# Kernel optimization log

Hardware: AMD Instinct MI355X
Metric: run time of the kernel (lower is better)

## Reference

```python
import jax, jax.numpy as jnp
import numpy as np

N = 100000      # nodes
E = 1600000     # edges (before self-loops)
F_IN = 128      # dataset.num_node_features
H, C = 8, 8     # heads, hid
D = H * C       # 64, concat output dim
G = 64          # graphs in batch
N_CLS = 10
SLOPE = 0.2     # PyG GATConv negative_slope default


def setup_inputs() -> dict:
    key = jax.random.key(0)
    ks = jax.random.split(key, 16)
    s = 0.1
    return {
        "x": jax.random.normal(ks[0], (N, F_IN), jnp.float32),
        "edge_index": jax.random.randint(ks[1], (2, E), 0, N, jnp.int32),
        "batch": jnp.sort(jax.random.randint(ks[2], (N,), 0, G, jnp.int32)),
        "W1": jax.random.normal(ks[3], (F_IN, D), jnp.float32) * s,
        "a1_src": jax.random.normal(ks[4], (H, C), jnp.float32) * s,
        "a1_dst": jax.random.normal(ks[5], (H, C), jnp.float32) * s,
        "b1": jnp.zeros((D,), jnp.float32),
        "W2": jax.random.normal(ks[6], (D, D), jnp.float32) * s,
        "a2_src": jax.random.normal(ks[7], (H, C), jnp.float32) * s,
        "a2_dst": jax.random.normal(ks[8], (H, C), jnp.float32) * s,
        "b2": jnp.zeros((D,), jnp.float32),
        "W3": jax.random.normal(ks[9], (D, D), jnp.float32) * s,
        "a3_src": jax.random.normal(ks[10], (H, C), jnp.float32) * s,
        "a3_dst": jax.random.normal(ks[11], (H, C), jnp.float32) * s,
        "b3": jnp.zeros((D,), jnp.float32),
        "lin_W": jax.random.normal(ks[12], (D, N_CLS), jnp.float32) * s,
        "lin_b": jnp.zeros((N_CLS,), jnp.float32),
    }


def _gat_conv(h_in, src, dst, W, a_src, a_dst, b):
    # h: [N, H, C] per-head projected features
    h = (h_in @ W).reshape(N, H, C)
    al_src = jnp.einsum('nhc,hc->nh', h, a_src)  # [N, H]
    al_dst = jnp.einsum('nhc,hc->nh', h, a_dst)
    e = al_src[src] + al_dst[dst]                # [E', H]
    e = jnp.where(e > 0, e, SLOPE * e)           # LeakyReLU
    # segment softmax over incoming edges of each dst node
    m = jax.ops.segment_max(e, dst, num_segments=N)          # every node has a self-loop
    e = jnp.exp(e - m[dst])
    denom = jax.ops.segment_sum(e, dst, num_segments=N)
    alpha = e / denom[dst]                        # [E', H]
    out = jax.ops.segment_sum(h[src] * alpha[:, :, None], dst, num_segments=N)
    return out.reshape(N, D) + b


def reference(x, edge_index, batch, W1, a1_src, a1_dst, b1,
              W2, a2_src, a2_dst, b2, W3, a3_src, a3_dst, b3, lin_W, lin_b):
    # PyG GATConv add_self_loops=True
    loop = jnp.arange(N, dtype=edge_index.dtype)
    src = jnp.concatenate([edge_index[0], loop])
    dst = jnp.concatenate([edge_index[1], loop])

    h = jax.nn.elu(_gat_conv(x, src, dst, W1, a1_src, a1_dst, b1))
    h = jax.nn.elu(_gat_conv(h, src, dst, W2, a2_src, a2_dst, b2))
    h = jax.nn.elu(_gat_conv(h, src, dst, W3, a3_src, a3_dst, b3))

    # global mean pool over graph assignment
    sums = jax.ops.segment_sum(h, batch, num_segments=G)          # [G, D]
    cnts = jax.ops.segment_sum(jnp.ones((N,), h.dtype), batch, num_segments=G)
    pooled = sums / jnp.maximum(cnts, 1.0)[:, None]

    return pooled @ lin_W + lin_b  # [G, N_CLS]
```

## Files before the change

### kernel.cpp

```cpp
#include <hip/hip_runtime.h>
#include <math.h>

#define NN 100000
#define EE 1600000
#define GG 64
#define NCLS 10

#define BSH 8
#define NB 391
#define BCAP 4608
#define EPS 4096
#define CAPS 5120

typedef unsigned int uint32;

__device__ __forceinline__ unsigned short f2bf(float f) {
    unsigned u = __float_as_uint(f);
    unsigned r = (u + 0x7fffu + ((u >> 16) & 1u)) >> 16;
    return (unsigned short)r;
}


__global__ __launch_bounds__(512) void bscatter_kernel(
    const int* __restrict__ src, const int* __restrict__ dst,
    int* __restrict__ bfill, uint32* __restrict__ bpack, int n) {
    __shared__ int hist[512], gbase[512], lbase[512], cnt2[512];
    __shared__ int wtot[8];
    __shared__ uint32 lsd[EPS];
    __shared__ unsigned short bkt[EPS];
    int tid = threadIdx.x;
    int lane = tid & 63, wv = tid >> 6;
    int e0 = blockIdx.x * EPS;
    int e1 = min(e0 + EPS, n);

    hist[tid] = 0;
    cnt2[tid] = 0;
    __syncthreads();
    for (int e = e0 + tid; e < e1; e += 512) atomicAdd(&hist[dst[e] >> BSH], 1);
    __syncthreads();
    int h = hist[tid];
    int inc = h;
#pragma unroll
    for (int off = 1; off < 64; off <<= 1) {
        int t = __shfl_up(inc, off);
        if (lane >= off) inc += t;
    }
    if (lane == 63) wtot[wv] = inc;
    __syncthreads();
    if (tid < 8) {
        int t = wtot[tid];
#pragma unroll
        for (int off = 1; off < 8; off <<= 1) {
            int u = __shfl_up(t, off, 8);
            if (tid >= off) t += u;
        }
        wtot[tid] = t;
    }
    __syncthreads();
    if (wv > 0) inc += wtot[wv - 1];
    int lb = inc - h;
    lbase[tid] = lb;
    int go = h > 0 ? atomicAdd(&bfill[tid], h) : 0;
    gbase[tid] = tid * BCAP + go - lb;
    __syncthreads();
    for (int e = e0 + tid; e < e1; e += 512) {
        int s = src[e], dd = dst[e];
        int b = dd >> BSH;
        int r = atomicAdd(&cnt2[b], 1);
        int slot = lbase[b] + r;
        lsd[slot] = ((uint32)s << 8) | (uint32)(dd & 255);
        bkt[slot] = (unsigned short)b;
    }
    __syncthreads();
    int m = e1 - e0;
    for (int i = tid; i < m; i += 512)
        bpack[gbase[bkt[i]] + i] = lsd[i];
}

__global__ __launch_bounds__(256) void bsort_kernel(
    const uint32* __restrict__ bpack, const int* __restrict__ bfill,
    int* __restrict__ rp, int* __restrict__ re, int* __restrict__ col) {
    __shared__ int cnt[256], cnt2[256];
    __shared__ int wtot[4];
    __shared__ int stage[CAPS];
    int b = blockIdx.x;
    int tid = threadIdx.x;
    int ebeg = b * BCAP;
    int sz = bfill[b];
    int n0 = b << BSH;
    int nn = min(256, NN - n0);

    cnt[tid] = 0;
    cnt2[tid] = 0;
    __syncthreads();
    const uint4* bq = (const uint4*)(bpack + ebeg);
    int nq = sz >> 2;
    for (int i = tid; i < nq; i += 256) {
        uint4 p = bq[i];
        atomicAdd(&cnt[p.x & 255u], 1);
        atomicAdd(&cnt[p.y & 255u], 1);
        atomicAdd(&cnt[p.z & 255u], 1);
        atomicAdd(&cnt[p.w & 255u], 1);
    }
    for (int e = (nq << 2) + tid; e < sz; e += 256)
        atomicAdd(&cnt[bpack[ebeg + e] & 255u], 1);
    __syncthreads();
    int lane = tid & 63, wv = tid >> 6;
    int c = cnt[tid];
    int inc = c;
#pragma unroll
    for (int off = 1; off < 64; off <<= 1) {
        int t = __shfl_up(inc, off);
        if (lane >= off) inc += t;
    }
    if (lane == 63) wtot[wv] = inc;
    __syncthreads();
    if (tid < 4) {
        int t = wtot[tid];
#pragma unroll
        for (int off = 1; off < 4; off <<= 1) {
            int u = __shfl_up(t, off, 4);
            if (tid >= off) t += u;
        }
        wtot[tid] = t;
    }
    __syncthreads();
    if (wv > 0) inc += wtot[wv - 1];
    int excl = inc - c;
    cnt[tid] = excl;
    if (tid < nn) {
        rp[n0 + tid] = ebeg + excl;
        re[n0 + tid] = ebeg + inc;
    }
    __syncthreads();
    bool fits = sz <= CAPS;
    for (int i = tid; i < nq; i += 256) {
        uint4 p = bq[i];
        int d0 = (int)(p.x & 255u), d1 = (int)(p.y & 255u);
        int d2 = (int)(p.z & 255u), d3 = (int)(p.w & 255u);
        int p0 = cnt[d0] + atomicAdd(&cnt2[d0], 1);
        int p1 = cnt[d1] + atomicAdd(&cnt2[d1], 1);
        int p2 = cnt[d2] + atomicAdd(&cnt2[d2], 1);
        int p3 = cnt[d3] + atomicAdd(&cnt2[d3], 1);
        if (fits) {
            stage[p0] = (int)(p.x >> 8); stage[p1] = (int)(p.y >> 8);
            stage[p2] = (int)(p.z >> 8); stage[p3] = (int)(p.w >> 8);
        } else {
            col[ebeg + p0] = (int)(p.x >> 8); col[ebeg + p1] = (int)(p.y >> 8);
            col[ebeg + p2] = (int)(p.z >> 8); col[ebeg + p3] = (int)(p.w >> 8);
        }
    }
    for (int e = (nq << 2) + tid; e < sz; e += 256) {
        uint32 p = bpack[ebeg + e];
        int dl = (int)(p & 255u);
        int pos = cnt[dl] + atomicAdd(&cnt2[dl], 1);
        if (fits) stage[pos] = (int)(p >> 8);
        else col[ebeg + pos] = (int)(p >> 8);
    }
    __syncthreads();
    if (fits) {
        uint4* colq = (uint4*)(col + ebeg);
        const uint4* stq = (const uint4*)stage;
        for (int i = tid; i < nq; i += 256) colq[i] = stq[i];
        for (int i = (nq << 2) + tid; i < sz; i += 256) col[ebeg + i] = stage[i];
    }
}


template <int K>
__global__ __launch_bounds__(256) void gemm_al_kernel(
    const float* __restrict__ X, const float* __restrict__ W,
    const float* __restrict__ a_src, const float* __restrict__ a_dst,
    unsigned short* __restrict__ H, float* __restrict__ ALs, float* __restrict__ ALd,
    int nrows) {
    const int KC = 64;
    const int KP = KC + 4;
    __shared__ float Xs[64 * (KC + 4)];
    __shared__ float Ws[K * 64];
    int tid = threadIdx.x;
    int r0 = blockIdx.x * 64;
    int validRows = min(64, nrows - r0);

    {
        const float4* Wg = (const float4*)W;
        float4* Ws4 = (float4*)Ws;
        for (int i = tid; i < K * 16; i += 256) Ws4[i] = Wg[i];
    }

    int cg = tid & 15, rg = tid >> 4;
    int rbase = rg * 4;
    float4 acc0 = make_float4(0.f, 0.f, 0.f, 0.f);
    float4 acc1 = acc0, acc2 = acc0, acc3 = acc0;

    const float4* Xg = (const float4*)X;
    const int QG = K / 4;

    for (int kc = 0; kc < K; kc += KC) {
        __syncthreads();
        for (int i = tid; i < 64 * 16; i += 256) {
            int row = i >> 4, q = i & 15;
            float4 v = (row < validRows)
                ? Xg[(size_t)(r0 + row) * QG + (kc >> 2) + q]
                : make_float4(0.f, 0.f, 0.f, 0.f);
            *(float4*)&Xs[row * KP + q * 4] = v;
        }
        __syncthreads();

#pragma unroll 2
        for (int k = 0; k < KC; k += 4) {
            float4 x0 = *(const float4*)&Xs[(rbase + 0) * KP + k];
            float4 x1 = *(const float4*)&Xs[(rbase + 1) * KP + k];
            float4 x2 = *(const float4*)&Xs[(rbase + 2) * KP + k];
            float4 x3 = *(const float4*)&Xs[(rbase + 3) * KP + k];
            float4 w0 = *(const float4*)&Ws[(kc + k + 0) * 64 + 4 * cg];
            float4 w1 = *(const float4*)&Ws[(kc + k + 1) * 64 + 4 * cg];
            float4 w2 = *(const float4*)&Ws[(kc + k + 2) * 64 + 4 * cg];
            float4 w3 = *(const float4*)&Ws[(kc + k + 3) * 64 + 4 * cg];
#define FMA4(A, S, WV) \
            A.x = fmaf(S, WV.x, A.x); A.y = fmaf(S, WV.y, A.y); \
            A.z = fmaf(S, WV.z, A.z); A.w = fmaf(S, WV.w, A.w)
            FMA4(acc0, x0.x, w0); FMA4(acc1, x1.x, w0); FMA4(acc2, x2.x, w0); FMA4(acc3, x3.x, w0);
            FMA4(acc0, x0.y, w1); FMA4(acc1, x1.y, w1); FMA4(acc2, x2.y, w1); FMA4(acc3, x3.y, w1);
            FMA4(acc0, x0.z, w2); FMA4(acc1, x1.z, w2); FMA4(acc2, x2.z, w2); FMA4(acc3, x3.z, w2);
            FMA4(acc0, x0.w, w3); FMA4(acc1, x1.w, w3); FMA4(acc2, x2.w, w3); FMA4(acc3, x3.w, w3);
#undef FMA4
        }
    }

    int hh = cg >> 1;
    float4 as4 = ((const float4*)a_src)[cg];
    float4 ad4 = ((const float4*)a_dst)[cg];
    float4 accs[4] = {acc0, acc1, acc2, acc3};
#pragma unroll
    for (int i = 0; i < 4; ++i) {
        int r = r0 + rbase + i;
        if (r < nrows) {
            ushort4 p;
            p.x = f2bf(accs[i].x); p.y = f2bf(accs[i].y);
            p.z = f2bf(accs[i].z); p.w = f2bf(accs[i].w);
            ((ushort4*)H)[(size_t)r * 16 + cg] = p;
            float ps = accs[i].x * as4.x + accs[i].y * as4.y +
                       accs[i].z * as4.z + accs[i].w * as4.w;
            float pd = accs[i].x * ad4.x + accs[i].y * ad4.y +
                       accs[i].z * ad4.z + accs[i].w * ad4.w;
            ps += __shfl_xor(ps, 1);
            pd += __shfl_xor(pd, 1);
            if ((cg & 1) == 0) {
                ALs[r * 8 + hh] = ps;
                ALd[r * 8 + hh] = pd;
            }
        }
    }
}


__global__ __launch_bounds__(256, 6) void agg_kernel(
    const unsigned short* __restrict__ H, const float* __restrict__ ALs,
    const float* __restrict__ ALd, const int* __restrict__ rp,
    const int* __restrict__ re, const int* __restrict__ col,
    const float* __restrict__ bias, float* __restrict__ Out, int n) {
    int tid = threadIdx.x;
    int lane = tid & 63;
    int slot = lane >> 3, head = lane & 7;
    int wid = blockIdx.x * 4 + (tid >> 6);
    int d = wid * 8 + slot;
    bool active = d < n;
    if (!active) d = n - 1;
    const uint4* __restrict__ Hq = (const uint4*)H;

    float ad = ALd[d * 8 + head];
    float acc0 = 0.f, acc1 = 0.f, acc2 = 0.f, acc3 = 0.f;
    float acc4 = 0.f, acc5 = 0.f, acc6 = 0.f, acc7 = 0.f;
    float wsum = 0.f;

#define FMA8(U, W) { \
    acc0 = fmaf(W, __uint_as_float((U).x << 16), acc0); \
    acc1 = fmaf(W, __uint_as_float((U).x & 0xffff0000u), acc1); \
    acc2 = fmaf(W, __uint_as_float((U).y << 16), acc2); \
    acc3 = fmaf(W, __uint_as_float((U).y & 0xffff0000u), acc3); \
    acc4 = fmaf(W, __uint_as_float((U).z << 16), acc4); \
    acc5 = fmaf(W, __uint_as_float((U).z & 0xffff0000u), acc5); \
    acc6 = fmaf(W, __uint_as_float((U).w << 16), acc6); \
    acc7 = fmaf(W, __uint_as_float((U).w & 0xffff0000u), acc7); }

    {
        uint4 u = Hq[(size_t)d * 8 + head];
        float e = ALs[d * 8 + head] + ad;
        e = fmaxf(e, 0.2f * e);
        float w = __expf(e);
        FMA8(u, w);
        wsum = w;
    }

    int k = rp[d], kend = re[d];
    for (; k + 4 <= kend; k += 4) {
        int s0 = col[k], s1 = col[k + 1], s2 = col[k + 2], s3 = col[k + 3];
        uint4 u0 = Hq[(size_t)s0 * 8 + head];
        uint4 u1 = Hq[(size_t)s1 * 8 + head];
        uint4 u2 = Hq[(size_t)s2 * 8 + head];
        uint4 u3 = Hq[(size_t)s3 * 8 + head];
        float a0 = ALs[s0 * 8 + head];
        float a1 = ALs[s1 * 8 + head];
        float a2 = ALs[s2 * 8 + head];
        float a3 = ALs[s3 * 8 + head];
        float e0 = a0 + ad; e0 = fmaxf(e0, 0.2f * e0); float w0 = __expf(e0);
        float e1 = a1 + ad; e1 = fmaxf(e1, 0.2f * e1); float w1 = __expf(e1);
        float e2 = a2 + ad; e2 = fmaxf(e2, 0.2f * e2); float w2 = __expf(e2);
        float e3 = a3 + ad; e3 = fmaxf(e3, 0.2f * e3); float w3 = __expf(e3);
        FMA8(u0, w0);
        FMA8(u1, w1);
        FMA8(u2, w2);
        FMA8(u3, w3);
        wsum += (w0 + w1) + (w2 + w3);
    }
    if (k + 2 <= kend) {
        int s0 = col[k], s1 = col[k + 1];
        uint4 u0 = Hq[(size_t)s0 * 8 + head];
        uint4 u1 = Hq[(size_t)s1 * 8 + head];
        float a0 = ALs[s0 * 8 + head];
        float a1 = ALs[s1 * 8 + head];
        float e0 = a0 + ad; e0 = fmaxf(e0, 0.2f * e0); float w0 = __expf(e0);
        float e1 = a1 + ad; e1 = fmaxf(e1, 0.2f * e1); float w1 = __expf(e1);
        FMA8(u0, w0);
        FMA8(u1, w1);
        wsum += w0 + w1;
        k += 2;
    }
    if (k < kend) {
        int s = col[k];
        uint4 u = Hq[(size_t)s * 8 + head];
        float a = ALs[s * 8 + head];
        float e = a + ad; e = fmaxf(e, 0.2f * e);
        float w = __expf(e);
        FMA8(u, w);
        wsum += w;
    }
#undef FMA8

    if (active) {
        float inv = 1.f / wsum;
        float4 b0 = ((const float4*)bias)[head * 2];
        float4 b1 = ((const float4*)bias)[head * 2 + 1];
        float4 o0, o1;
        o0.x = fmaf(acc0, inv, b0.x); o0.x = o0.x > 0.f ? o0.x : expm1f(o0.x);
        o0.y = fmaf(acc1, inv, b0.y); o0.y = o0.y > 0.f ? o0.y : expm1f(o0.y);
        o0.z = fmaf(acc2, inv, b0.z); o0.z = o0.z > 0.f ? o0.z : expm1f(o0.z);
        o0.w = fmaf(acc3, inv, b0.w); o0.w = o0.w > 0.f ? o0.w : expm1f(o0.w);
        o1.x = fmaf(acc4, inv, b1.x); o1.x = o1.x > 0.f ? o1.x : expm1f(o1.x);
        o1.y = fmaf(acc5, inv, b1.y); o1.y = o1.y > 0.f ? o1.y : expm1f(o1.y);
        o1.z = fmaf(acc6, inv, b1.z); o1.z = o1.z > 0.f ? o1.z : expm1f(o1.z);
        o1.w = fmaf(acc7, inv, b1.w); o1.w = o1.w > 0.f ? o1.w : expm1f(o1.w);
        ((float4*)Out)[(size_t)d * 16 + head * 2] = o0;
        ((float4*)Out)[(size_t)d * 16 + head * 2 + 1] = o1;
    }
}


__global__ void pool_kernel(const float* __restrict__ H, const int* __restrict__ batch,
                            float* __restrict__ sums, float* __restrict__ cnt, int n) {
    int gw = (int)((blockIdx.x * blockDim.x + threadIdx.x) >> 6);
    int lane = threadIdx.x & 63;
    int n0 = gw * 64;
    if (n0 >= n) return;
    int n1 = min(n0 + 64, n);
    int curb = batch[n0];
    float local = 0.f, c_local = 0.f;
    for (int i = n0; i < n1; ++i) {
        int b = batch[i];
        if (b != curb) {
            atomicAdd(&sums[curb * 64 + lane], local);
            if (lane == 0) atomicAdd(&cnt[curb], c_local);
            local = 0.f;
            c_local = 0.f;
            curb = b;
        }
        local += H[(size_t)i * 64 + lane];
        c_local += 1.f;
    }
    atomicAdd(&sums[curb * 64 + lane], local);
    if (lane == 0) atomicAdd(&cnt[curb], c_local);
}

__global__ void final_kernel(const float* __restrict__ sums, const float* __restrict__ cnt,
                             const float* __restrict__ W, const float* __restrict__ b,
                             float* __restrict__ out) {
    int t = blockIdx.x * blockDim.x + threadIdx.x;
    if (t >= GG * NCLS) return;
    int g = t / NCLS, k = t % NCLS;
    float c = cnt[g];
    if (c < 1.f) c = 1.f;
    float inv = 1.f / c;
    float acc = b[k];
#pragma unroll
    for (int cc = 0; cc < 64; ++cc)
        acc = fmaf(sums[g * 64 + cc] * inv, W[cc * NCLS + k], acc);
    out[t] = acc;
}


extern "C" void kernel_launch(void* const* d_in, const int* in_sizes, int n_in,
                              void* d_out, int out_size, void* d_ws, size_t ws_size,
                              hipStream_t stream) {
    const float* x    = (const float*)d_in[0];
    const int*   ei   = (const int*)d_in[1];
    const int*   batch = (const int*)d_in[2];
    const float* W1 = (const float*)d_in[3];
    const float* a1s = (const float*)d_in[4];
    const float* a1d = (const float*)d_in[5];
    const float* b1 = (const float*)d_in[6];
    const float* W2 = (const float*)d_in[7];
    const float* a2s = (const float*)d_in[8];
    const float* a2d = (const float*)d_in[9];
    const float* b2 = (const float*)d_in[10];
    const float* W3 = (const float*)d_in[11];
    const float* a3s = (const float*)d_in[12];
    const float* a3d = (const float*)d_in[13];
    const float* b3 = (const float*)d_in[14];
    const float* linW = (const float*)d_in[15];
    const float* linb = (const float*)d_in[16];
    float* out = (float*)d_out;

    char* ws = (char*)d_ws;
    size_t off = 0;
    auto alloc = [&](size_t bytes) -> void* {
        void* p = ws + off;
        off = (off + bytes + 255) & ~(size_t)255;
        return p;
    };
    unsigned short* hBf = (unsigned short*)alloc((size_t)NN * 64 * 2);
    float* hF     = (float*)alloc((size_t)NN * 64 * 4);
    float* ALs    = (float*)alloc((size_t)NN * 8 * 4);
    float* ALd    = (float*)alloc((size_t)NN * 8 * 4);
    int*   rp     = (int*)alloc((size_t)NN * 4);
    int*   reArr  = (int*)alloc((size_t)NN * 4);
    int*   bfill  = (int*)alloc((size_t)NB * 4);
    uint32* bpack = (uint32*)alloc((size_t)NB * BCAP * 4);
    int*   col    = (int*)alloc((size_t)NB * BCAP * 4);
    float* sums   = (float*)alloc((size_t)(GG * 64 + GG) * 4);
    float* gcnt   = sums + GG * 64;

    const int NBLK = (NN + 255) / 256;
    const int SB = (EE + EPS - 1) / EPS;

    hipMemsetAsync(bfill, 0, (size_t)NB * 4, stream);
    bscatter_kernel<<<SB, 512, 0, stream>>>(ei, ei + EE, bfill, bpack, EE);
    bsort_kernel<<<NB, 256, 0, stream>>>(bpack, bfill, rp, reArr, col);

    const int GB = (NN + 63) / 64;
    const int AB = (NN + 31) / 32;

    gemm_al_kernel<128><<<GB, 256, 0, stream>>>(x, W1, a1s, a1d, hBf, ALs, ALd, NN);
    agg_kernel<<<AB, 256, 0, stream>>>(hBf, ALs, ALd, rp, reArr, col, b1, hF, NN);

    gemm_al_kernel<64><<<GB, 256, 0, stream>>>(hF, W2, a2s, a2d, hBf, ALs, ALd, NN);
    agg_kernel<<<AB, 256, 0, stream>>>(hBf, ALs, ALd, rp, reArr, col, b2, hF, NN);

    gemm_al_kernel<64><<<GB, 256, 0, stream>>>(hF, W3, a3s, a3d, hBf, ALs, ALd, NN);
    agg_kernel<<<AB, 256, 0, stream>>>(hBf, ALs, ALd, rp, reArr, col, b3, hF, NN);

    hipMemsetAsync(sums, 0, (size_t)(GG * 64 + GG) * 4, stream);
    pool_kernel<<<NBLK, 256, 0, stream>>>(hF, batch, sums, gcnt, NN);
    final_kernel<<<3, 256, 0, stream>>>(sums, gcnt, linW, linb, out);
}
```

Measured before the change: 395.7 us.

## Fuse aggregation with next-layer GEMM, merge scatter with first GEMM, fuse pooling

The edge bucket scatter and the first-layer projection GEMM now run as one launch, with blocks partitioned by role so they can overlap. Each layer's attention aggregation writes its ELU output into shared memory, and the next layer's projection and attention logits are computed from it, so the fp32 hidden tensor no longer round-trips through global memory. The last layer fuses aggregation with mean pooling and uses a last-block ticket to run the final linear layer. Row pointers are packed into int2, and H/AL buffers are ping-ponged between layers. Fewer launches and less memory traffic are traded for lower occupancy in the fused blocks (more shared memory per block) and atomic ticket synchronisation.

```diff
diff --git a/kernel.cpp b/kernel.cpp
--- a/kernel.cpp
+++ b/kernel.cpp
@@ -11,6 +11,8 @@
 #define BCAP 4608
 #define EPS 4096
 #define CAPS 5120
+#define SBLK 391
+#define GB 1563
 
 typedef unsigned int uint32;
 
@@ -21,253 +23,11 @@
 }
 
 
-__global__ __launch_bounds__(512) void bscatter_kernel(
-    const int* __restrict__ src, const int* __restrict__ dst,
-    int* __restrict__ bfill, uint32* __restrict__ bpack, int n) {
-    __shared__ int hist[512], gbase[512], lbase[512], cnt2[512];
-    __shared__ int wtot[8];
-    __shared__ uint32 lsd[EPS];
-    __shared__ unsigned short bkt[EPS];
-    int tid = threadIdx.x;
-    int lane = tid & 63, wv = tid >> 6;
-    int e0 = blockIdx.x * EPS;
-    int e1 = min(e0 + EPS, n);
-
-    hist[tid] = 0;
-    cnt2[tid] = 0;
-    __syncthreads();
-    for (int e = e0 + tid; e < e1; e += 512) atomicAdd(&hist[dst[e] >> BSH], 1);
-    __syncthreads();
-    int h = hist[tid];
-    int inc = h;
-#pragma unroll
-    for (int off = 1; off < 64; off <<= 1) {
-        int t = __shfl_up(inc, off);
-        if (lane >= off) inc += t;
-    }
-    if (lane == 63) wtot[wv] = inc;
-    __syncthreads();
-    if (tid < 8) {
-        int t = wtot[tid];
-#pragma unroll
-        for (int off = 1; off < 8; off <<= 1) {
-            int u = __shfl_up(t, off, 8);
-            if (tid >= off) t += u;
-        }
-        wtot[tid] = t;
-    }
-    __syncthreads();
-    if (wv > 0) inc += wtot[wv - 1];
-    int lb = inc - h;
-    lbase[tid] = lb;
-    int go = h > 0 ? atomicAdd(&bfill[tid], h) : 0;
-    gbase[tid] = tid * BCAP + go - lb;
-    __syncthreads();
-    for (int e = e0 + tid; e < e1; e += 512) {
-        int s = src[e], dd = dst[e];
-        int b = dd >> BSH;
-        int r = atomicAdd(&cnt2[b], 1);
-        int slot = lbase[b] + r;
-        lsd[slot] = ((uint32)s << 8) | (uint32)(dd & 255);
-        bkt[slot] = (unsigned short)b;
-    }
-    __syncthreads();
-    int m = e1 - e0;
-    for (int i = tid; i < m; i += 512)
-        bpack[gbase[bkt[i]] + i] = lsd[i];
-}
-
-__global__ __launch_bounds__(256) void bsort_kernel(
-    const uint32* __restrict__ bpack, const int* __restrict__ bfill,
-    int* __restrict__ rp, int* __restrict__ re, int* __restrict__ col) {
-    __shared__ int cnt[256], cnt2[256];
-    __shared__ int wtot[4];
-    __shared__ int stage[CAPS];
-    int b = blockIdx.x;
-    int tid = threadIdx.x;
-    int ebeg = b * BCAP;
-    int sz = bfill[b];
-    int n0 = b << BSH;
-    int nn = min(256, NN - n0);
-
-    cnt[tid] = 0;
-    cnt2[tid] = 0;
-    __syncthreads();
-    const uint4* bq = (const uint4*)(bpack + ebeg);
-    int nq = sz >> 2;
-    for (int i = tid; i < nq; i += 256) {
-        uint4 p = bq[i];
-        atomicAdd(&cnt[p.x & 255u], 1);
-        atomicAdd(&cnt[p.y & 255u], 1);
-        atomicAdd(&cnt[p.z & 255u], 1);
-        atomicAdd(&cnt[p.w & 255u], 1);
-    }
-    for (int e = (nq << 2) + tid; e < sz; e += 256)
-        atomicAdd(&cnt[bpack[ebeg + e] & 255u], 1);
-    __syncthreads();
-    int lane = tid & 63, wv = tid >> 6;
-    int c = cnt[tid];
-    int inc = c;
-#pragma unroll
-    for (int off = 1; off < 64; off <<= 1) {
-        int t = __shfl_up(inc, off);
-        if (lane >= off) inc += t;
-    }
-    if (lane == 63) wtot[wv] = inc;
-    __syncthreads();
-    if (tid < 4) {
-        int t = wtot[tid];
-#pragma unroll
-        for (int off = 1; off < 4; off <<= 1) {
-            int u = __shfl_up(t, off, 4);
-            if (tid >= off) t += u;
-        }
-        wtot[tid] = t;
-    }
-    __syncthreads();
-    if (wv > 0) inc += wtot[wv - 1];
-    int excl = inc - c;
-    cnt[tid] = excl;
-    if (tid < nn) {
-        rp[n0 + tid] = ebeg + excl;
-        re[n0 + tid] = ebeg + inc;
-    }
-    __syncthreads();
-    bool fits = sz <= CAPS;
-    for (int i = tid; i < nq; i += 256) {
-        uint4 p = bq[i];
-        int d0 = (int)(p.x & 255u), d1 = (int)(p.y & 255u);
-        int d2 = (int)(p.z & 255u), d3 = (int)(p.w & 255u);
-        int p0 = cnt[d0] + atomicAdd(&cnt2[d0], 1);
-        int p1 = cnt[d1] + atomicAdd(&cnt2[d1], 1);
-        int p2 = cnt[d2] + atomicAdd(&cnt2[d2], 1);
-        int p3 = cnt[d3] + atomicAdd(&cnt2[d3], 1);
-        if (fits) {
-            stage[p0] = (int)(p.x >> 8); stage[p1] = (int)(p.y >> 8);
-            stage[p2] = (int)(p.z >> 8); stage[p3] = (int)(p.w >> 8);
-        } else {
-            col[ebeg + p0] = (int)(p.x >> 8); col[ebeg + p1] = (int)(p.y >> 8);
-            col[ebeg + p2] = (int)(p.z >> 8); col[ebeg + p3] = (int)(p.w >> 8);
-        }
-    }
-    for (int e = (nq << 2) + tid; e < sz; e += 256) {
-        uint32 p = bpack[ebeg + e];
-        int dl = (int)(p & 255u);
-        int pos = cnt[dl] + atomicAdd(&cnt2[dl], 1);
-        if (fits) stage[pos] = (int)(p >> 8);
-        else col[ebeg + pos] = (int)(p >> 8);
-    }
-    __syncthreads();
-    if (fits) {
-        uint4* colq = (uint4*)(col + ebeg);
-        const uint4* stq = (const uint4*)stage;
-        for (int i = tid; i < nq; i += 256) colq[i] = stq[i];
-        for (int i = (nq << 2) + tid; i < sz; i += 256) col[ebeg + i] = stage[i];
-    }
-}
-
-
-template <int K>
-__global__ __launch_bounds__(256) void gemm_al_kernel(
-    const float* __restrict__ X, const float* __restrict__ W,
-    const float* __restrict__ a_src, const float* __restrict__ a_dst,
-    unsigned short* __restrict__ H, float* __restrict__ ALs, float* __restrict__ ALd,
-    int nrows) {
-    const int KC = 64;
-    const int KP = KC + 4;
-    __shared__ float Xs[64 * (KC + 4)];
-    __shared__ float Ws[K * 64];
-    int tid = threadIdx.x;
-    int r0 = blockIdx.x * 64;
-    int validRows = min(64, nrows - r0);
-
-    {
-        const float4* Wg = (const float4*)W;
-        float4* Ws4 = (float4*)Ws;
-        for (int i = tid; i < K * 16; i += 256) Ws4[i] = Wg[i];
-    }
-
-    int cg = tid & 15, rg = tid >> 4;
-    int rbase = rg * 4;
-    float4 acc0 = make_float4(0.f, 0.f, 0.f, 0.f);
-    float4 acc1 = acc0, acc2 = acc0, acc3 = acc0;
-
-    const float4* Xg = (const float4*)X;
-    const int QG = K / 4;
-
-    for (int kc = 0; kc < K; kc += KC) {
-        __syncthreads();
-        for (int i = tid; i < 64 * 16; i += 256) {
-            int row = i >> 4, q = i & 15;
-            float4 v = (row < validRows)
-                ? Xg[(size_t)(r0 + row) * QG + (kc >> 2) + q]
-                : make_float4(0.f, 0.f, 0.f, 0.f);
-            *(float4*)&Xs[row * KP + q * 4] = v;
-        }
-        __syncthreads();
-
-#pragma unroll 2
-        for (int k = 0; k < KC; k += 4) {
-            float4 x0 = *(const float4*)&Xs[(rbase + 0) * KP + k];
-            float4 x1 = *(const float4*)&Xs[(rbase + 1) * KP + k];
-            float4 x2 = *(const float4*)&Xs[(rbase + 2) * KP + k];
-            float4 x3 = *(const float4*)&Xs[(rbase + 3) * KP + k];
-            float4 w0 = *(const float4*)&Ws[(kc + k + 0) * 64 + 4 * cg];
-            float4 w1 = *(const float4*)&Ws[(kc + k + 1) * 64 + 4 * cg];
-            float4 w2 = *(const float4*)&Ws[(kc + k + 2) * 64 + 4 * cg];
-            float4 w3 = *(const float4*)&Ws[(kc + k + 3) * 64 + 4 * cg];
-#define FMA4(A, S, WV) \
-            A.x = fmaf(S, WV.x, A.x); A.y = fmaf(S, WV.y, A.y); \
-            A.z = fmaf(S, WV.z, A.z); A.w = fmaf(S, WV.w, A.w)
-            FMA4(acc0, x0.x, w0); FMA4(acc1, x1.x, w0); FMA4(acc2, x2.x, w0); FMA4(acc3, x3.x, w0);
-            FMA4(acc0, x0.y, w1); FMA4(acc1, x1.y, w1); FMA4(acc2, x2.y, w1); FMA4(acc3, x3.y, w1);
-            FMA4(acc0, x0.z, w2); FMA4(acc1, x1.z, w2); FMA4(acc2, x2.z, w2); FMA4(acc3, x3.z, w2);
-            FMA4(acc0, x0.w, w3); FMA4(acc1, x1.w, w3); FMA4(acc2, x2.w, w3); FMA4(acc3, x3.w, w3);
-#undef FMA4
-        }
-    }
-
-    int hh = cg >> 1;
-    float4 as4 = ((const float4*)a_src)[cg];
-    float4 ad4 = ((const float4*)a_dst)[cg];
-    float4 accs[4] = {acc0, acc1, acc2, acc3};
-#pragma unroll
-    for (int i = 0; i < 4; ++i) {
-        int r = r0 + rbase + i;
-        if (r < nrows) {
-            ushort4 p;
-            p.x = f2bf(accs[i].x); p.y = f2bf(accs[i].y);
-            p.z = f2bf(accs[i].z); p.w = f2bf(accs[i].w);
-            ((ushort4*)H)[(size_t)r * 16 + cg] = p;
-            float ps = accs[i].x * as4.x + accs[i].y * as4.y +
-                       accs[i].z * as4.z + accs[i].w * as4.w;
-            float pd = accs[i].x * ad4.x + accs[i].y * ad4.y +
-                       accs[i].z * ad4.z + accs[i].w * ad4.w;
-            ps += __shfl_xor(ps, 1);
-            pd += __shfl_xor(pd, 1);
-            if ((cg & 1) == 0) {
-                ALs[r * 8 + hh] = ps;
-                ALd[r * 8 + hh] = pd;
-            }
-        }
-    }
-}
-
-
-__global__ __launch_bounds__(256, 6) void agg_kernel(
-    const unsigned short* __restrict__ H, const float* __restrict__ ALs,
-    const float* __restrict__ ALd, const int* __restrict__ rp,
-    const int* __restrict__ re, const int* __restrict__ col,
-    const float* __restrict__ bias, float* __restrict__ Out, int n) {
-    int tid = threadIdx.x;
-    int lane = tid & 63;
-    int slot = lane >> 3, head = lane & 7;
-    int wid = blockIdx.x * 4 + (tid >> 6);
-    int d = wid * 8 + slot;
-    bool active = d < n;
-    if (!active) d = n - 1;
-    const uint4* __restrict__ Hq = (const uint4*)H;
-
+__device__ __forceinline__ void agg_node(
+    const uint4* __restrict__ Hq, const float* __restrict__ ALs,
+    const float* __restrict__ ALd, const int2* __restrict__ rpe,
+    const int* __restrict__ col, const float* __restrict__ bias,
+    int d, int head, float* __restrict__ out8) {
     float ad = ALd[d * 8 + head];
     float acc0 = 0.f, acc1 = 0.f, acc2 = 0.f, acc3 = 0.f;
     float acc4 = 0.f, acc5 = 0.f, acc6 = 0.f, acc7 = 0.f;
@@ -292,7 +52,8 @@
         wsum = w;
     }
 
-    int k = rp[d], kend = re[d];
+    int2 kk = rpe[d];
+    int k = kk.x, kend = kk.y;
     for (; k + 4 <= kend; k += 4) {
         int s0 = col[k], s1 = col[k + 1], s2 = col[k + 2], s3 = col[k + 3];
         uint4 u0 = Hq[(size_t)s0 * 8 + head];
@@ -337,64 +98,416 @@
     }
 #undef FMA8
 
-    if (active) {
-        float inv = 1.f / wsum;
-        float4 b0 = ((const float4*)bias)[head * 2];
-        float4 b1 = ((const float4*)bias)[head * 2 + 1];
-        float4 o0, o1;
-        o0.x = fmaf(acc0, inv, b0.x); o0.x = o0.x > 0.f ? o0.x : expm1f(o0.x);
-        o0.y = fmaf(acc1, inv, b0.y); o0.y = o0.y > 0.f ? o0.y : expm1f(o0.y);
-        o0.z = fmaf(acc2, inv, b0.z); o0.z = o0.z > 0.f ? o0.z : expm1f(o0.z);
-        o0.w = fmaf(acc3, inv, b0.w); o0.w = o0.w > 0.f ? o0.w : expm1f(o0.w);
-        o1.x = fmaf(acc4, inv, b1.x); o1.x = o1.x > 0.f ? o1.x : expm1f(o1.x);
-        o1.y = fmaf(acc5, inv, b1.y); o1.y = o1.y > 0.f ? o1.y : expm1f(o1.y);
-        o1.z = fmaf(acc6, inv, b1.z); o1.z = o1.z > 0.f ? o1.z : expm1f(o1.z);
-        o1.w = fmaf(acc7, inv, b1.w); o1.w = o1.w > 0.f ? o1.w : expm1f(o1.w);
-        ((float4*)Out)[(size_t)d * 16 + head * 2] = o0;
-        ((float4*)Out)[(size_t)d * 16 + head * 2 + 1] = o1;
-    }
-}
-
-
-__global__ void pool_kernel(const float* __restrict__ H, const int* __restrict__ batch,
-                            float* __restrict__ sums, float* __restrict__ cnt, int n) {
-    int gw = (int)((blockIdx.x * blockDim.x + threadIdx.x) >> 6);
-    int lane = threadIdx.x & 63;
-    int n0 = gw * 64;
-    if (n0 >= n) return;
-    int n1 = min(n0 + 64, n);
-    int curb = batch[n0];
-    float local = 0.f, c_local = 0.f;
-    for (int i = n0; i < n1; ++i) {
-        int b = batch[i];
-        if (b != curb) {
-            atomicAdd(&sums[curb * 64 + lane], local);
-            if (lane == 0) atomicAdd(&cnt[curb], c_local);
-            local = 0.f;
-            c_local = 0.f;
-            curb = b;
-        }
-        local += H[(size_t)i * 64 + lane];
-        c_local += 1.f;
-    }
-    atomicAdd(&sums[curb * 64 + lane], local);
-    if (lane == 0) atomicAdd(&cnt[curb], c_local);
-}
-
-__global__ void final_kernel(const float* __restrict__ sums, const float* __restrict__ cnt,
-                             const float* __restrict__ W, const float* __restrict__ b,
-                             float* __restrict__ out) {
-    int t = blockIdx.x * blockDim.x + threadIdx.x;
-    if (t >= GG * NCLS) return;
-    int g = t / NCLS, k = t % NCLS;
-    float c = cnt[g];
-    if (c < 1.f) c = 1.f;
-    float inv = 1.f / c;
-    float acc = b[k];
-#pragma unroll
-    for (int cc = 0; cc < 64; ++cc)
-        acc = fmaf(sums[g * 64 + cc] * inv, W[cc * NCLS + k], acc);
-    out[t] = acc;
+    float inv = 1.f / wsum;
+    float4 b0 = ((const float4*)bias)[head * 2];
+    float4 b1 = ((const float4*)bias)[head * 2 + 1];
+    float4 o0, o1;
+    o0.x = fmaf(acc0, inv, b0.x); o0.x = o0.x > 0.f ? o0.x : expm1f(o0.x);
+    o0.y = fmaf(acc1, inv, b0.y); o0.y = o0.y > 0.f ? o0.y : expm1f(o0.y);
+    o0.z = fmaf(acc2, inv, b0.z); o0.z = o0.z > 0.f ? o0.z : expm1f(o0.z);
+    o0.w = fmaf(acc3, inv, b0.w); o0.w = o0.w > 0.f ? o0.w : expm1f(o0.w);
+    o1.x = fmaf(acc4, inv, b1.x); o1.x = o1.x > 0.f ? o1.x : expm1f(o1.x);
+    o1.y = fmaf(acc5, inv, b1.y); o1.y = o1.y > 0.f ? o1.y : expm1f(o1.y);
+    o1.z = fmaf(acc6, inv, b1.z); o1.z = o1.z > 0.f ? o1.z : expm1f(o1.z);
+    o1.w = fmaf(acc7, inv, b1.w); o1.w = o1.w > 0.f ? o1.w : expm1f(o1.w);
+    ((float4*)out8)[0] = o0;
+    ((float4*)out8)[1] = o1;
+}
+
+
+__global__ __launch_bounds__(512) void pre_kernel(
+    const int* __restrict__ src, const int* __restrict__ dst,
+    int* __restrict__ bfill, uint32* __restrict__ bpack, int nE,
+    const float* __restrict__ X, const float* __restrict__ W,
+    const float* __restrict__ a_src, const float* __restrict__ a_dst,
+    unsigned short* __restrict__ H, float* __restrict__ ALs, float* __restrict__ ALd) {
+    __shared__ __align__(16) char smem[50176];
+    int tid = threadIdx.x;
+
+    if (blockIdx.x < SBLK) {
+        int* hist  = (int*)smem;
+        int* gbase = hist + 512;
+        int* lbase = gbase + 512;
+        int* cnt2  = lbase + 512;
+        int* wtot  = cnt2 + 512;
+        uint32* lsd = (uint32*)(wtot + 8);
+        unsigned short* bkt = (unsigned short*)(lsd + EPS);
+
+        int lane = tid & 63, wv = tid >> 6;
+        int e0 = blockIdx.x * EPS;
+        int e1 = min(e0 + EPS, nE);
+
+        hist[tid] = 0;
+        cnt2[tid] = 0;
+        __syncthreads();
+        for (int e = e0 + tid; e < e1; e += 512) atomicAdd(&hist[dst[e] >> BSH], 1);
+        __syncthreads();
+        int h = hist[tid];
+        int inc = h;
+#pragma unroll
+        for (int off = 1; off < 64; off <<= 1) {
+            int t = __shfl_up(inc, off);
+            if (lane >= off) inc += t;
+        }
+        if (lane == 63) wtot[wv] = inc;
+        __syncthreads();
+        if (tid < 8) {
+            int t = wtot[tid];
+#pragma unroll
+            for (int off = 1; off < 8; off <<= 1) {
+                int u = __shfl_up(t, off, 8);
+                if (tid >= off) t += u;
+            }
+            wtot[tid] = t;
+        }
+        __syncthreads();
+        if (wv > 0) inc += wtot[wv - 1];
+        int lb = inc - h;
+        lbase[tid] = lb;
+        int go = h > 0 ? atomicAdd(&bfill[tid], h) : 0;
+        gbase[tid] = tid * BCAP + go - lb;
+        __syncthreads();
+        for (int e = e0 + tid; e < e1; e += 512) {
+            int s = src[e], dd = dst[e];
+            int b = dd >> BSH;
+            int r = atomicAdd(&cnt2[b], 1);
+            int slot = lbase[b] + r;
+            lsd[slot] = ((uint32)s << 8) | (uint32)(dd & 255);
+            bkt[slot] = (unsigned short)b;
+        }
+        __syncthreads();
+        int m = e1 - e0;
+        for (int i = tid; i < m; i += 512)
+            bpack[gbase[bkt[i]] + i] = lsd[i];
+    } else {
+        const int K = 128, KC = 64, KP = 68;
+        float* Xs = (float*)smem;
+        float* Ws = Xs + 64 * KP;
+        int r0 = (blockIdx.x - SBLK) * 64;
+        int validRows = min(64, NN - r0);
+
+        {
+            const float4* Wg = (const float4*)W;
+            float4* Ws4 = (float4*)Ws;
+            for (int i = tid; i < K * 16; i += 512) Ws4[i] = Wg[i];
+        }
+
+        int cg = tid & 15, rg = tid >> 4;
+        int rbase = rg * 2;
+        float4 acc0 = make_float4(0.f, 0.f, 0.f, 0.f);
+        float4 acc1 = acc0;
+
+        const float4* Xg = (const float4*)X;
+        const int QG = K / 4;
+
+        for (int kc = 0; kc < K; kc += KC) {
+            __syncthreads();
+            for (int i = tid; i < 64 * 16; i += 512) {
+                int row = i >> 4, q = i & 15;
+                float4 v = (row < validRows)
+                    ? Xg[(size_t)(r0 + row) * QG + (kc >> 2) + q]
+                    : make_float4(0.f, 0.f, 0.f, 0.f);
+                *(float4*)&Xs[row * KP + q * 4] = v;
+            }
+            __syncthreads();
+
+#pragma unroll 2
+            for (int k = 0; k < KC; k += 4) {
+                float4 x0 = *(const float4*)&Xs[(rbase + 0) * KP + k];
+                float4 x1 = *(const float4*)&Xs[(rbase + 1) * KP + k];
+                float4 w0 = *(const float4*)&Ws[(kc + k + 0) * 64 + 4 * cg];
+                float4 w1 = *(const float4*)&Ws[(kc + k + 1) * 64 + 4 * cg];
+                float4 w2 = *(const float4*)&Ws[(kc + k + 2) * 64 + 4 * cg];
+                float4 w3 = *(const float4*)&Ws[(kc + k + 3) * 64 + 4 * cg];
+#define FMA4(A, S, WV) \
+                A.x = fmaf(S, WV.x, A.x); A.y = fmaf(S, WV.y, A.y); \
+                A.z = fmaf(S, WV.z, A.z); A.w = fmaf(S, WV.w, A.w)
+                FMA4(acc0, x0.x, w0); FMA4(acc1, x1.x, w0);
+                FMA4(acc0, x0.y, w1); FMA4(acc1, x1.y, w1);
+                FMA4(acc0, x0.z, w2); FMA4(acc1, x1.z, w2);
+                FMA4(acc0, x0.w, w3); FMA4(acc1, x1.w, w3);
+#undef FMA4
+            }
+        }
+
+        int hh = cg >> 1;
+        float4 as4 = ((const float4*)a_src)[cg];
+        float4 ad4 = ((const float4*)a_dst)[cg];
+        float4 accs[2] = {acc0, acc1};
+#pragma unroll
+        for (int i = 0; i < 2; ++i) {
+            int r = r0 + rbase + i;
+            if (r < NN) {
+                ushort4 p;
+                p.x = f2bf(accs[i].x); p.y = f2bf(accs[i].y);
+                p.z = f2bf(accs[i].z); p.w = f2bf(accs[i].w);
+                ((ushort4*)H)[(size_t)r * 16 + cg] = p;
+                float ps = accs[i].x * as4.x + accs[i].y * as4.y +
+                           accs[i].z * as4.z + accs[i].w * as4.w;
+                float pd = accs[i].x * ad4.x + accs[i].y * ad4.y +
+                           accs[i].z * ad4.z + accs[i].w * ad4.w;
+                ps += __shfl_xor(ps, 1);
+                pd += __shfl_xor(pd, 1);
+                if ((cg & 1) == 0) {
+                    ALs[r * 8 + hh] = ps;
+                    ALd[r * 8 + hh] = pd;
+                }
+            }
+        }
+    }
+}
+
+
+__global__ __launch_bounds__(256) void bsort_kernel(
+    const uint32* __restrict__ bpack, const int* __restrict__ bfill,
+    int2* __restrict__ rpe, int* __restrict__ col) {
+    __shared__ int cnt[256], cnt2[256];
+    __shared__ int wtot[4];
+    __shared__ int stage[CAPS];
+    int b = blockIdx.x;
+    int tid = threadIdx.x;
+    int ebeg = b * BCAP;
+    int sz = bfill[b];
+    int n0 = b << BSH;
+    int nn = min(256, NN - n0);
+
+    cnt[tid] = 0;
+    cnt2[tid] = 0;
+    __syncthreads();
+    const uint4* bq = (const uint4*)(bpack + ebeg);
+    int nq = sz >> 2;
+    for (int i = tid; i < nq; i += 256) {
+        uint4 p = bq[i];
+        atomicAdd(&cnt[p.x & 255u], 1);
+        atomicAdd(&cnt[p.y & 255u], 1);
+        atomicAdd(&cnt[p.z & 255u], 1);
+        atomicAdd(&cnt[p.w & 255u], 1);
+    }
+    for (int e = (nq << 2) + tid; e < sz; e += 256)
+        atomicAdd(&cnt[bpack[ebeg + e] & 255u], 1);
+    __syncthreads();
+    int lane = tid & 63, wv = tid >> 6;
+    int c = cnt[tid];
+    int inc = c;
+#pragma unroll
+    for (int off = 1; off < 64; off <<= 1) {
+        int t = __shfl_up(inc, off);
+        if (lane >= off) inc += t;
+    }
+    if (lane == 63) wtot[wv] = inc;
+    __syncthreads();
+    if (tid < 4) {
+        int t = wtot[tid];
+#pragma unroll
+        for (int off = 1; off < 4; off <<= 1) {
+            int u = __shfl_up(t, off, 4);
+            if (tid >= off) t += u;
+        }
+        wtot[tid] = t;
+    }
+    __syncthreads();
+    if (wv > 0) inc += wtot[wv - 1];
+    int excl = inc - c;
+    cnt[tid] = excl;
+    if (tid < nn) {
+        rpe[n0 + tid] = make_int2(ebeg + excl, ebeg + inc);
+    }
+    __syncthreads();
+    bool fits = sz <= CAPS;
+    for (int i = tid; i < nq; i += 256) {
+        uint4 p = bq[i];
+        int d0 = (int)(p.x & 255u), d1 = (int)(p.y & 255u);
+        int d2 = (int)(p.z & 255u), d3 = (int)(p.w & 255u);
+        int p0 = cnt[d0] + atomicAdd(&cnt2[d0], 1);
+        int p1 = cnt[d1] + atomicAdd(&cnt2[d1], 1);
+        int p2 = cnt[d2] + atomicAdd(&cnt2[d2], 1);
+        int p3 = cnt[d3] + atomicAdd(&cnt2[d3], 1);
+        if (fits) {
+            stage[p0] = (int)(p.x >> 8); stage[p1] = (int)(p.y >> 8);
+            stage[p2] = (int)(p.z >> 8); stage[p3] = (int)(p.w >> 8);
+        } else {
+            col[ebeg + p0] = (int)(p.x >> 8); col[ebeg + p1] = (int)(p.y >> 8);
+            col[ebeg + p2] = (int)(p.z >> 8); col[ebeg + p3] = (int)(p.w >> 8);
+        }
+    }
+    for (int e = (nq << 2) + tid; e < sz; e += 256) {
+        uint32 p = bpack[ebeg + e];
+        int dl = (int)(p & 255u);
+        int pos = cnt[dl] + atomicAdd(&cnt2[dl], 1);
+        if (fits) stage[pos] = (int)(p >> 8);
+        else col[ebeg + pos] = (int)(p >> 8);
+    }
+    __syncthreads();
+    if (fits) {
+        uint4* colq = (uint4*)(col + ebeg);
+        const uint4* stq = (const uint4*)stage;
+        for (int i = tid; i < nq; i += 256) colq[i] = stq[i];
+        for (int i = (nq << 2) + tid; i < sz; i += 256) col[ebeg + i] = stage[i];
+    }
+}
+
+
+__global__ __launch_bounds__(256) void layer_kernel(
+    const unsigned short* __restrict__ Hin, const float* __restrict__ ALsIn,
+    const float* __restrict__ ALdIn, const int2* __restrict__ rpe,
+    const int* __restrict__ col, const float* __restrict__ biasIn,
+    const float* __restrict__ Wn, const float* __restrict__ ansrc,
+    const float* __restrict__ andst, unsigned short* __restrict__ Hout,
+    float* __restrict__ ALsOut, float* __restrict__ ALdOut, int n) {
+    const int KP = 68;
+    __shared__ float Xs[64 * KP];
+    __shared__ float Ws[64 * 64];
+    int tid = threadIdx.x;
+    int r0 = blockIdx.x * 64;
+    int validRows = min(64, n - r0);
+
+    {
+        const float4* Wg = (const float4*)Wn;
+        float4* Ws4 = (float4*)Ws;
+        for (int i = tid; i < 64 * 16; i += 256) Ws4[i] = Wg[i];
+    }
+    if (validRows < 64) {
+        for (int i = tid; i < 64 * KP; i += 256) Xs[i] = 0.f;
+        __syncthreads();
+    }
+
+    int lane = tid & 63, wv = tid >> 6;
+    int slot = lane >> 3, head = lane & 7;
+    const uint4* Hq = (const uint4*)Hin;
+#pragma unroll
+    for (int pass = 0; pass < 2; ++pass) {
+        int row = pass * 32 + wv * 8 + slot;
+        int d = r0 + row;
+        if (d < n)
+            agg_node(Hq, ALsIn, ALdIn, rpe, col, biasIn, d, head, &Xs[row * KP + head * 8]);
+    }
+    __syncthreads();
+
+    int cg = tid & 15, rg = tid >> 4;
+    int rbase = rg * 4;
+    float4 acc0 = make_float4(0.f, 0.f, 0.f, 0.f);
+    float4 acc1 = acc0, acc2 = acc0, acc3 = acc0;
+#pragma unroll 2
+    for (int k = 0; k < 64; k += 4) {
+        float4 x0 = *(const float4*)&Xs[(rbase + 0) * KP + k];
+        float4 x1 = *(const float4*)&Xs[(rbase + 1) * KP + k];
+        float4 x2 = *(const float4*)&Xs[(rbase + 2) * KP + k];
+        float4 x3 = *(const float4*)&Xs[(rbase + 3) * KP + k];
+        float4 w0 = *(const float4*)&Ws[(k + 0) * 64 + 4 * cg];
+        float4 w1 = *(const float4*)&Ws[(k + 1) * 64 + 4 * cg];
+        float4 w2 = *(const float4*)&Ws[(k + 2) * 64 + 4 * cg];
+        float4 w3 = *(const float4*)&Ws[(k + 3) * 64 + 4 * cg];
+#define FMA4(A, S, WV) \
+        A.x = fmaf(S, WV.x, A.x); A.y = fmaf(S, WV.y, A.y); \
+        A.z = fmaf(S, WV.z, A.z); A.w = fmaf(S, WV.w, A.w)
+        FMA4(acc0, x0.x, w0); FMA4(acc1, x1.x, w0); FMA4(acc2, x2.x, w0); FMA4(acc3, x3.x, w0);
+        FMA4(acc0, x0.y, w1); FMA4(acc1, x1.y, w1); FMA4(acc2, x2.y, w1); FMA4(acc3, x3.y, w1);
+        FMA4(acc0, x0.z, w2); FMA4(acc1, x1.z, w2); FMA4(acc2, x2.z, w2); FMA4(acc3, x3.z, w2);
+        FMA4(acc0, x0.w, w3); FMA4(acc1, x1.w, w3); FMA4(acc2, x2.w, w3); FMA4(acc3, x3.w, w3);
+#undef FMA4
+    }
+
+    int hh = cg >> 1;
+    float4 as4 = ((const float4*)ansrc)[cg];
+    float4 ad4 = ((const float4*)andst)[cg];
+    float4 accs[4] = {acc0, acc1, acc2, acc3};
+#pragma unroll
+    for (int i = 0; i < 4; ++i) {
+        int r = r0 + rbase + i;
+        if (r < n) {
+            ushort4 p;
+            p.x = f2bf(accs[i].x); p.y = f2bf(accs[i].y);
+            p.z = f2bf(accs[i].z); p.w = f2bf(accs[i].w);
+            ((ushort4*)Hout)[(size_t)r * 16 + cg] = p;
+            float ps = accs[i].x * as4.x + accs[i].y * as4.y +
+                       accs[i].z * as4.z + accs[i].w * as4.w;
+            float pd = accs[i].x * ad4.x + accs[i].y * ad4.y +
+                       accs[i].z * ad4.z + accs[i].w * ad4.w;
+            ps += __shfl_xor(ps, 1);
+            pd += __shfl_xor(pd, 1);
+            if ((cg & 1) == 0) {
+                ALsOut[r * 8 + hh] = ps;
+                ALdOut[r * 8 + hh] = pd;
+            }
+        }
+    }
+}
+
+
+__global__ __launch_bounds__(256) void last_kernel(
+    const unsigned short* __restrict__ Hin, const float* __restrict__ ALsIn,
+    const float* __restrict__ ALdIn, const int2* __restrict__ rpe,
+    const int* __restrict__ col, const float* __restrict__ biasIn,
+    const int* __restrict__ batch, float* __restrict__ sums,
+    float* __restrict__ gcnt, int* __restrict__ ticket,
+    const float* __restrict__ linW, const float* __restrict__ linb,
+    float* __restrict__ out, int n) {
+    const int KP = 68;
+    __shared__ float Xs[64 * KP];
+    __shared__ int lflag;
+    int tid = threadIdx.x;
+    int r0 = blockIdx.x * 64;
+    int validRows = min(64, n - r0);
+
+    if (validRows < 64) {
+        for (int i = tid; i < 64 * KP; i += 256) Xs[i] = 0.f;
+        __syncthreads();
+    }
+
+    int lane = tid & 63, wv = tid >> 6;
+    int slot = lane >> 3, head = lane & 7;
+    const uint4* Hq = (const uint4*)Hin;
+#pragma unroll
+    for (int pass = 0; pass < 2; ++pass) {
+        int row = pass * 32 + wv * 8 + slot;
+        int d = r0 + row;
+        if (d < n)
+            agg_node(Hq, ALsIn, ALdIn, rpe, col, biasIn, d, head, &Xs[row * KP + head * 8]);
+    }
+    __syncthreads();
+
+    int f = tid & 63, q = tid >> 6;
+    int rbeg = q * 16, rend = min(rbeg + 16, validRows);
+    if (rbeg < rend) {
+        int curb = batch[r0 + rbeg];
+        float loc = 0.f, c = 0.f;
+        for (int row = rbeg; row < rend; ++row) {
+            int b = batch[r0 + row];
+            if (b != curb) {
+                atomicAdd(&sums[curb * 64 + f], loc);
+                if (f == 0) atomicAdd(&gcnt[curb], c);
+                loc = 0.f; c = 0.f; curb = b;
+            }
+            loc += Xs[row * KP + f];
+            c += 1.f;
+        }
+        atomicAdd(&sums[curb * 64 + f], loc);
+        if (f == 0) atomicAdd(&gcnt[curb], c);
+    }
+
+    __threadfence();
+    __syncthreads();
+    if (tid == 0) {
+        int t = __hip_atomic_fetch_add(ticket, 1, __ATOMIC_ACQ_REL, __HIP_MEMORY_SCOPE_AGENT);
+        lflag = (t == (int)gridDim.x - 1) ? 1 : 0;
+    }
+    __syncthreads();
+    if (lflag) {
+        for (int t2 = tid; t2 < GG * NCLS; t2 += 256) {
+            int g = t2 / NCLS, k = t2 % NCLS;
+            float c = __hip_atomic_load(&gcnt[g], __ATOMIC_RELAXED, __HIP_MEMORY_SCOPE_AGENT);
+            if (c < 1.f) c = 1.f;
+            float inv = 1.f / c;
+            float acc = linb[k];
+#pragma unroll
+            for (int cc = 0; cc < 64; ++cc) {
+                float s = __hip_atomic_load(&sums[g * 64 + cc], __ATOMIC_RELAXED,
+                                            __HIP_MEMORY_SCOPE_AGENT);
+                acc = fmaf(s * inv, linW[cc * NCLS + k], acc);
+            }
+            out[t2] = acc;
+        }
+    }
 }
 
 
@@ -427,38 +540,33 @@
         off = (off + bytes + 255) & ~(size_t)255;
         return p;
     };
-    unsigned short* hBf = (unsigned short*)alloc((size_t)NN * 64 * 2);
-    float* hF     = (float*)alloc((size_t)NN * 64 * 4);
-    float* ALs    = (float*)alloc((size_t)NN * 8 * 4);
-    float* ALd    = (float*)alloc((size_t)NN * 8 * 4);
-    int*   rp     = (int*)alloc((size_t)NN * 4);
-    int*   reArr  = (int*)alloc((size_t)NN * 4);
-    int*   bfill  = (int*)alloc((size_t)NB * 4);
+    const size_t ZBYTES = (size_t)NB * 4 + (size_t)GG * 64 * 4 + (size_t)GG * 4 + 4;
+    char* zr = (char*)alloc(ZBYTES);
+    int*   bfill = (int*)zr;
+    float* sums  = (float*)(zr + (size_t)NB * 4);
+    float* gcnt  = sums + GG * 64;
+    int*   ticket = (int*)(gcnt + GG);
+
+    unsigned short* hA = (unsigned short*)alloc((size_t)NN * 64 * 2);
+    unsigned short* hB = (unsigned short*)alloc((size_t)NN * 64 * 2);
+    float* ALsA = (float*)alloc((size_t)NN * 8 * 4);
+    float* ALdA = (float*)alloc((size_t)NN * 8 * 4);
+    float* ALsB = (float*)alloc((size_t)NN * 8 * 4);
+    float* ALdB = (float*)alloc((size_t)NN * 8 * 4);
+    int2*  rpe  = (int2*)alloc((size_t)NN * 8);
     uint32* bpack = (uint32*)alloc((size_t)NB * BCAP * 4);
-    int*   col    = (int*)alloc((size_t)NB * BCAP * 4);
-    float* sums   = (float*)alloc((size_t)(GG * 64 + GG) * 4);
-    float* gcnt   = sums + GG * 64;
-
-    const int NBLK = (NN + 255) / 256;
-    const int SB = (EE + EPS - 1) / EPS;
-
-    hipMemsetAsync(bfill, 0, (size_t)NB * 4, stream);
-    bscatter_kernel<<<SB, 512, 0, stream>>>(ei, ei + EE, bfill, bpack, EE);
-    bsort_kernel<<<NB, 256, 0, stream>>>(bpack, bfill, rp, reArr, col);
-
-    const int GB = (NN + 63) / 64;
-    const int AB = (NN + 31) / 32;
-
-    gemm_al_kernel<128><<<GB, 256, 0, stream>>>(x, W1, a1s, a1d, hBf, ALs, ALd, NN);
-    agg_kernel<<<AB, 256, 0, stream>>>(hBf, ALs, ALd, rp, reArr, col, b1, hF, NN);
-
-    gemm_al_kernel<64><<<GB, 256, 0, stream>>>(hF, W2, a2s, a2d, hBf, ALs, ALd, NN);
-    agg_kernel<<<AB, 256, 0, stream>>>(hBf, ALs, ALd, rp, reArr, col, b2, hF, NN);
-
-    gemm_al_kernel<64><<<GB, 256, 0, stream>>>(hF, W3, a3s, a3d, hBf, ALs, ALd, NN);
-    agg_kernel<<<AB, 256, 0, stream>>>(hBf, ALs, ALd, rp, reArr, col, b3, hF, NN);
-
-    hipMemsetAsync(sums, 0, (size_t)(GG * 64 + GG) * 4, stream);
-    pool_kernel<<<NBLK, 256, 0, stream>>>(hF, batch, sums, gcnt, NN);
-    final_kernel<<<3, 256, 0, stream>>>(sums, gcnt, linW, linb, out);
-}
+    int*   col  = (int*)alloc((size_t)NB * BCAP * 4);
+
+    hipMemsetAsync(zr, 0, ZBYTES, stream);
+
+    pre_kernel<<<SBLK + GB, 512, 0, stream>>>(ei, ei + EE, bfill, bpack, EE,
+                                              x, W1, a1s, a1d, hA, ALsA, ALdA);
+    bsort_kernel<<<NB, 256, 0, stream>>>(bpack, bfill, rpe, col);
+
+    layer_kernel<<<GB, 256, 0, stream>>>(hA, ALsA, ALdA, rpe, col, b1,
+                                         W2, a2s, a2d, hB, ALsB, ALdB, NN);
+    layer_kernel<<<GB, 256, 0, stream>>>(hB, ALsB, ALdB, rpe, col, b2,
+                                         W3, a3s, a3d, hA, ALsA, ALdA, NN);
+    last_kernel<<<GB, 256, 0, stream>>>(hA, ALsA, ALdA, rpe, col, b3,
+                                        batch, sums, gcnt, ticket, linW, linb, out, NN);
+}
```

Result: slower. 465.8 us (+17.7%).
